# Performance work log

Hardware: AMD Instinct MI355X
Metric: run time of the kernel (lower is better)

## Reference

```python
import jax, jax.numpy as jnp
import numpy as np

NUM_HEADS = 16
D_MODEL = 1024
NUM_LAYERS = 4
VOCAB = 32000
SEQ_LEN = 1024
BATCH = 4
EPS = 1e-6


def position_embedding(seq_len, d_model):
    pos = jnp.arange(seq_len, dtype=jnp.float32)[:, None]
    i = jnp.arange(d_model, dtype=jnp.float32)[None, :]
    # faithful to source: angle_rates = 1 / (1/10000)^(2*(i//2)/d) = 10000^(2*(i//2)/d)
    angle_rates = jnp.power(10000.0, 2.0 * jnp.floor(i / 2.0) / float(d_model))
    ang = pos * angle_rates  # [S, D]
    return jnp.concatenate([jnp.sin(ang[:, 0::2]), jnp.cos(ang[:, 1::2])], axis=-1)[None]  # [1,S,D]


def layer_norm(x, g, b):
    m = jnp.mean(x, axis=-1, keepdims=True)
    v = jnp.mean(jnp.square(x - m), axis=-1, keepdims=True)
    return (x - m) * jax.lax.rsqrt(v + EPS) * g + b


def setup_inputs() -> dict:
    key = jax.random.key(0)
    ks = jax.random.split(key, 20)
    L, D = NUM_LAYERS, D_MODEL
    s = 0.02
    inp = {
        "x": jax.random.randint(ks[0], (BATCH, SEQ_LEN), 0, VOCAB, dtype=jnp.int32),
        "mask": jnp.zeros((BATCH, 1, 1, SEQ_LEN), dtype=jnp.float32),
        "emb": jax.random.normal(ks[1], (VOCAB, D), dtype=jnp.float32) * s,
        "wq": jax.random.normal(ks[2], (L, D, D), dtype=jnp.float32) * s,
        "bq": jnp.zeros((L, D), dtype=jnp.float32),
        "wk": jax.random.normal(ks[3], (L, D, D), dtype=jnp.float32) * s,
        "bk": jnp.zeros((L, D), dtype=jnp.float32),
        "wv": jax.random.normal(ks[4], (L, D, D), dtype=jnp.float32) * s,
        "bv": jnp.zeros((L, D), dtype=jnp.float32),
        "wo": jax.random.normal(ks[5], (L, D, D), dtype=jnp.float32) * s,
        "bo": jnp.zeros((L, D), dtype=jnp.float32),
        "wf": jax.random.normal(ks[6], (L, D, D), dtype=jnp.float32) * s,
        "bf": jnp.zeros((L, D), dtype=jnp.float32),
        "g1": jnp.ones((L, D), dtype=jnp.float32),
        "b1": jnp.zeros((L, D), dtype=jnp.float32),
        "g2": jnp.ones((L, D), dtype=jnp.float32),
        "b2": jnp.zeros((L, D), dtype=jnp.float32),
    }
    return inp


def encoder_forward(x, mask, emb, wq, bq, wk, bk, wv, bv, wo, bo, wf, bf, g1, b1, g2, b2):
    B, S = x.shape
    D = emb.shape[1]
    H = NUM_HEADS
    dh = D // H
    h = emb[x] * jnp.sqrt(jnp.float32(D))  # [B,S,D]
    h = h + position_embedding(S, D)[:, :S, :]

    def split_heads(t):  # [B,S,D] -> [B,H,S,dh]
        return t.reshape(B, S, H, dh).transpose(0, 2, 1, 3)

    for l in range(wq.shape[0]):
        q = split_heads(h @ wq[l] + bq[l])
        k = split_heads(h @ wk[l] + bk[l])
        v = split_heads(h @ wv[l] + bv[l])
        scores = jnp.einsum("bhqd,bhkd->bhqk", q, k) / jnp.sqrt(jnp.float32(dh))
        scores = scores + mask * -1e9
        w = jax.nn.softmax(scores, axis=-1)
        ctx = jnp.einsum("bhqk,bhkd->bhqd", w, v)  # [B,H,S,dh]
        ctx = ctx.transpose(0, 2, 1, 3).reshape(B, S, D)
        attn_out = ctx @ wo[l] + bo[l]
        h = layer_norm(h + attn_out, g1[l], b1[l])
        ff = h @ wf[l] + bf[l]
        h = layer_norm(h + ff, g2[l], b2[l])
    return h


def reference(x, mask, emb, wq, bq, wk, bk, wv, bv, wo, bo, wf, bf, g1, b1, g2, b2):
    return encoder_forward(x, mask, emb, wq, bq, wk, bk, wv, bv, wo, bo, wf, bf, g1, b1, g2, b2)
```

## Files before the change

kernel.cpp:

```cpp
#include <hip/hip_runtime.h>
#include <hip/hip_bf16.h>
#include <math.h>

typedef __hip_bfloat16 bf16;
typedef unsigned int u32;
typedef __attribute__((ext_vector_type(8))) short short8;
typedef __attribute__((ext_vector_type(4))) float f32x4;


#define ATT_LDK 72
#define PS_LD  72

typedef __attribute__((address_space(3))) u32 lds_u32;
typedef const __attribute__((address_space(1))) u32 glb_u32;
static __device__ __forceinline__ void g2l16(const void* g, void* l) {
    __builtin_amdgcn_global_load_lds((glb_u32*)g, (lds_u32*)l, 16, 0, 0);
}

static __device__ __forceinline__ unsigned short bf16bits(float f) {
    bf16 h = __float2bfloat16(f);
    return *(unsigned short*)&h;
}

__global__ __launch_bounds__(256) void wprep_kernel(
    const float* __restrict__ wq, const float* __restrict__ wk,
    const float* __restrict__ wv, const float* __restrict__ wo,
    const float* __restrict__ wf, bf16* __restrict__ wt_all)
{
    __shared__ bf16 tile[64][ATT_LDK];
    const int z = blockIdx.z;
    const int l = z / 5, f = z % 5;
    const float* src = (f == 0) ? wq : (f == 1) ? wk : (f == 2) ? wv : (f == 3) ? wo : wf;
    src += (size_t)l * 1024 * 1024;
    bf16* dst = wt_all + ((size_t)l * 5 + f) * 1024 * 1024;

    const int k0 = blockIdx.x * 64, n0 = blockIdx.y * 64;
    const int t = threadIdx.x;
#pragma unroll
    for (int rr = 0; rr < 4; ++rr) {
        int slot = t + rr * 256;
        int r = slot >> 4, c = slot & 15;
        float4 v = *(const float4*)(src + (size_t)(k0 + r) * 1024 + n0 + c * 4);
        tile[c * 4 + 0][r] = __float2bfloat16(v.x);
        tile[c * 4 + 1][r] = __float2bfloat16(v.y);
        tile[c * 4 + 2][r] = __float2bfloat16(v.z);
        tile[c * 4 + 3][r] = __float2bfloat16(v.w);
    }
    __syncthreads();
#pragma unroll
    for (int rr = 0; rr < 2; ++rr) {
        int slot = t + rr * 256;
        int n = slot >> 3, c = slot & 7;
        *(uint4*)(dst + (size_t)(n0 + n) * 1024 + k0 + c * 8) = *(const uint4*)&tile[n][c * 8];
    }
}

__global__ void bias_stack_kernel(const float* __restrict__ bq, const float* __restrict__ bk,
                                  const float* __restrict__ bv, float* __restrict__ bqkv)
{
    int i = blockIdx.x * 256 + threadIdx.x;
    if (i < 4 * 3072) {
        int l = i / 3072, c = i % 3072;
        int fam = c >> 10, cc = c & 1023;
        const float* s = (fam == 0) ? bq : (fam == 1) ? bk : bv;
        bqkv[i] = s[l * 1024 + cc];
    }
}

__global__ __launch_bounds__(256) void pe_kernel(float* __restrict__ pe)
{
    int idx = blockIdx.x * 256 + threadIdx.x;
    int d0 = (idx & 255) * 4;
    int s = idx >> 8;
    float out[4];
#pragma unroll
    for (int j = 0; j < 4; ++j) {
        int d = d0 + j;
        int m = (d < 512) ? d : (d - 512);
        float ex = (float)(2 * m) * (1.0f / 1024.0f);
        float rate = (float)pow(10000.0, (double)ex);
        float ang = (float)s * rate;
        double a = (double)ang;
        out[j] = (d < 512) ? (float)sin(a) : (float)cos(a);
    }
    *(float4*)(pe + (size_t)s * 1024 + d0) = *(float4*)out;
}

__global__ __launch_bounds__(256) void embed_kernel(
    const int* __restrict__ x, const float* __restrict__ emb,
    const float* __restrict__ pe,
    float* __restrict__ hf, bf16* __restrict__ hb)
{
    int idx = blockIdx.x * 256 + threadIdx.x;
    int d0 = (idx & 255) * 4;
    int row = idx >> 8;
    int s = row & 1023;
    int tok = x[row];
    float4 e = *(const float4*)(emb + (size_t)tok * 1024 + d0);
    float4 p = *(const float4*)(pe + (size_t)s * 1024 + d0);
    float out[4] = {e.x * 32.0f + p.x, e.y * 32.0f + p.y,
                    e.z * 32.0f + p.z, e.w * 32.0f + p.w};
    *(float4*)(hf + (size_t)row * 1024 + d0) = *(float4*)out;
    unsigned short pk[4];
#pragma unroll
    for (int j = 0; j < 4; ++j) pk[j] = bf16bits(out[j]);
    *(uint2*)(hb + (size_t)row * 1024 + d0) = *(uint2*)pk;
}

__global__ __launch_bounds__(256, 3) void gemm_bt_kernel(
    const bf16* __restrict__ A, const bf16* __restrict__ Bt,
    const float* __restrict__ bias,
    bf16* __restrict__ Cb, bf16* __restrict__ VtOut,
    int M, int N, int K)
{
    __shared__ bf16 As[2][128 * 32];
    __shared__ bf16 Bs[2][128 * 32];
    __shared__ bf16 Cst[4][16 * PS_LD];
    const int t = threadIdx.x;
    const int lane = t & 63, wave = t >> 6;
    const int wr = wave >> 1, wc = wave & 1;
    const int lidx = lane & 15, quad = lane >> 4;
    const int m0 = blockIdx.x * 128, n0 = blockIdx.y * 128;

    f32x4 acc[4][4];
#pragma unroll
    for (int i = 0; i < 4; ++i)
#pragma unroll
        for (int j = 0; j < 4; ++j) acc[i][j] = (f32x4){0.f, 0.f, 0.f, 0.f};

    const int r0 = wave * 32;
    const int rloc = lane >> 2;
    const int csw = ((lane & 3) ^ ((lane >> 3) & 3)) * 8;
    const bf16* Abase = A  + (size_t)(m0 + r0 + rloc) * K + csw;
    const bf16* Bbase = Bt + (size_t)(n0 + r0 + rloc) * K + csw;
    const int lofs = r0 * 32;
    const int aslot = (quad ^ ((lidx >> 1) & 3)) * 8;

    g2l16(Abase,                  &As[0][lofs]);
    g2l16(Abase + 16 * (size_t)K, &As[0][lofs + 16 * 32]);
    g2l16(Bbase,                  &Bs[0][lofs]);
    g2l16(Bbase + 16 * (size_t)K, &Bs[0][lofs + 16 * 32]);

    for (int k0 = 0; k0 < K; k0 += 32) {
        __syncthreads();
        const int cur = (k0 >> 5) & 1;
        if (k0 + 32 < K) {
            const int kn = k0 + 32;
            g2l16(Abase + kn,                  &As[cur ^ 1][lofs]);
            g2l16(Abase + kn + 16 * (size_t)K, &As[cur ^ 1][lofs + 16 * 32]);
            g2l16(Bbase + kn,                  &Bs[cur ^ 1][lofs]);
            g2l16(Bbase + kn + 16 * (size_t)K, &Bs[cur ^ 1][lofs + 16 * 32]);
        }

        short8 af[4], bfr[4];
#pragma unroll
        for (int i = 0; i < 4; ++i)
            af[i] = *(const short8*)(&As[cur][(wr * 64 + i * 16 + lidx) * 32 + aslot]);
#pragma unroll
        for (int j = 0; j < 4; ++j)
            bfr[j] = *(const short8*)(&Bs[cur][(wc * 64 + j * 16 + lidx) * 32 + aslot]);
#pragma unroll
        for (int i = 0; i < 4; ++i)
#pragma unroll
            for (int j = 0; j < 4; ++j)
                acc[i][j] = __builtin_amdgcn_mfma_f32_16x16x32_bf16(af[i], bfr[j], acc[i][j], 0, 0, 0);
    }

    float bvj[4];
#pragma unroll
    for (int j = 0; j < 4; ++j)
        bvj[j] = bias ? bias[n0 + wc * 64 + j * 16 + lidx] : 0.0f;

    if (VtOut && n0 >= 2048) {
        const int bidx = m0 >> 10;
        const int s_base = (m0 & 1023) + wr * 64 + quad * 4;
        const int d_base = (n0 - 2048) + wc * 64;
#pragma unroll
        for (int i = 0; i < 4; ++i)
#pragma unroll
            for (int j = 0; j < 4; ++j) {
                unsigned short pk[4];
#pragma unroll
                for (int r = 0; r < 4; ++r)
                    pk[r] = bf16bits(acc[i][j][r] + bvj[j]);
                bf16* dst = VtOut + ((size_t)bidx * 1024 + d_base + j * 16 + lidx) * 1024
                            + s_base + i * 16;
                *(uint2*)dst = *(const uint2*)pk;
            }
    } else {
        const int row16 = lane >> 2, c4 = lane & 3;
#pragma unroll
        for (int i = 0; i < 4; ++i) {
#pragma unroll
            for (int j = 0; j < 4; ++j)
#pragma unroll
                for (int r = 0; r < 4; ++r)
                    Cst[wave][(quad * 4 + r) * PS_LD + j * 16 + lidx] =
                        __float2bfloat16(acc[i][j][r] + bvj[j]);
            bf16* dst = Cb + (size_t)(m0 + wr * 64 + i * 16 + row16) * N + n0 + wc * 64;
            const bf16* srcr = &Cst[wave][row16 * PS_LD];
#pragma unroll
            for (int h = 0; h < 2; ++h)
                *(uint4*)(dst + (c4 + 4 * h) * 8) = *(const uint4*)(srcr + (c4 + 4 * h) * 8);
        }
    }
}

__global__ __launch_bounds__(256, 4) void gemm64_kernel(
    const bf16* __restrict__ A, const bf16* __restrict__ Bt,
    const float* __restrict__ bias, const float* __restrict__ resid,
    float* __restrict__ Cf,
    int M, int N, int K)
{
    __shared__ bf16 As[2][64 * 32];
    __shared__ bf16 Bs[2][128 * 32];
    const int t = threadIdx.x;
    const int lane = t & 63, wave = t >> 6;
    const int wr = wave >> 1, wc = wave & 1;
    const int lidx = lane & 15, quad = lane >> 4;
    const int m0 = blockIdx.x * 64, n0 = blockIdx.y * 128;

    f32x4 acc[2][4];
#pragma unroll
    for (int i = 0; i < 2; ++i)
#pragma unroll
        for (int j = 0; j < 4; ++j) acc[i][j] = (f32x4){0.f, 0.f, 0.f, 0.f};

    const int rloc = lane >> 2;
    const int csw = ((lane & 3) ^ ((lane >> 3) & 3)) * 8;
    const bf16* Abase = A  + (size_t)(m0 + wave * 16 + rloc) * K + csw;
    const bf16* Bbase = Bt + (size_t)(n0 + wave * 32 + rloc) * K + csw;
    const int alofs = wave * 16 * 32;
    const int blofs = wave * 32 * 32;
    const int aslot = (quad ^ ((lidx >> 1) & 3)) * 8;

    g2l16(Abase,                  &As[0][alofs]);
    g2l16(Bbase,                  &Bs[0][blofs]);
    g2l16(Bbase + 16 * (size_t)K, &Bs[0][blofs + 16 * 32]);

    for (int k0 = 0; k0 < K; k0 += 32) {
        __syncthreads();
        const int cur = (k0 >> 5) & 1;
        if (k0 + 32 < K) {
            const int kn = k0 + 32;
            g2l16(Abase + kn,                  &As[cur ^ 1][alofs]);
            g2l16(Bbase + kn,                  &Bs[cur ^ 1][blofs]);
            g2l16(Bbase + kn + 16 * (size_t)K, &Bs[cur ^ 1][blofs + 16 * 32]);
        }

        short8 af[2], bfr[4];
#pragma unroll
        for (int i = 0; i < 2; ++i)
            af[i] = *(const short8*)(&As[cur][(wr * 32 + i * 16 + lidx) * 32 + aslot]);
#pragma unroll
        for (int j = 0; j < 4; ++j)
            bfr[j] = *(const short8*)(&Bs[cur][(wc * 64 + j * 16 + lidx) * 32 + aslot]);
#pragma unroll
        for (int i = 0; i < 2; ++i)
#pragma unroll
            for (int j = 0; j < 4; ++j)
                acc[i][j] = __builtin_amdgcn_mfma_f32_16x16x32_bf16(af[i], bfr[j], acc[i][j], 0, 0, 0);
    }

#pragma unroll
    for (int i = 0; i < 2; ++i)
#pragma unroll
        for (int j = 0; j < 4; ++j) {
            int col = n0 + wc * 64 + j * 16 + lidx;
            float bv = bias[col];
#pragma unroll
            for (int r = 0; r < 4; ++r) {
                int rowg = m0 + wr * 32 + i * 16 + quad * 4 + r;
                Cf[(size_t)rowg * N + col] =
                    acc[i][j][r] + bv + resid[(size_t)rowg * N + col];
            }
        }
}

__global__ __launch_bounds__(512, 4) void attention_kernel(
    const bf16* __restrict__ QKV,
    const bf16* __restrict__ Vt,
    const float* __restrict__ mask,
    bf16* __restrict__ ctx)
{
    __shared__ bf16 Ks[2][64 * 64];
    __shared__ bf16 Vs[2][64 * 64];
    __shared__ bf16 Ps[8][16 * PS_LD];

    const int t = threadIdx.x, lane = t & 63, wave = t >> 6;
    const int quad = lane >> 4, lidx = lane & 15;
    const int b = blockIdx.x >> 4, hh = blockIdx.x & 15;
    const int q0 = blockIdx.y * 128 + wave * 16;

    const int r8 = lane >> 3;
    const int gc = ((lane & 7) ^ r8) * 8;
    const bf16* kg0 = QKV + (size_t)(b * 1024 + wave * 8 + r8) * 3072 + 1024 + hh * 64 + gc;
    const bf16* vg0 = Vt  + (size_t)(b * 1024 + hh * 64 + wave * 8 + r8) * 1024 + gc;
    const int lofs = wave * 8 * 64;

    short8 qf[2];
    {
        const bf16* qp = QKV + (size_t)(b * 1024 + q0 + lidx) * 3072 + hh * 64;
        qf[0] = *(const short8*)(qp + quad * 8);
        qf[1] = *(const short8*)(qp + 32 + quad * 8);
    }

    f32x4 Oacc[4];
#pragma unroll
    for (int nt = 0; nt < 4; ++nt) Oacc[nt] = (f32x4){0.f, 0.f, 0.f, 0.f};
    float psum[4] = {0.f, 0.f, 0.f, 0.f};

    const int fslot = lidx & 7;

    g2l16(kg0, &Ks[0][lofs]);
    g2l16(vg0, &Vs[0][lofs]);

    for (int kt = 0; kt < 16; ++kt) {
        __syncthreads();
        const int cur = kt & 1;
        if (kt < 15) {
            g2l16(kg0 + (size_t)(kt + 1) * 64 * 3072, &Ks[cur ^ 1][lofs]);
            g2l16(vg0 + (kt + 1) * 64,                &Vs[cur ^ 1][lofs]);
        }

        f32x4 sacc[4];
#pragma unroll
        for (int nt = 0; nt < 4; ++nt) sacc[nt] = (f32x4){0.f, 0.f, 0.f, 0.f};
#pragma unroll
        for (int kk = 0; kk < 2; ++kk)
#pragma unroll
            for (int nt = 0; nt < 4; ++nt) {
                short8 kf = *(const short8*)(&Ks[cur][(nt * 16 + lidx) * 64 + (((kk * 4 + quad) ^ fslot) * 8)]);
                sacc[nt] = __builtin_amdgcn_mfma_f32_16x16x32_bf16(qf[kk], kf, sacc[nt], 0, 0, 0);
            }

#pragma unroll
        for (int nt = 0; nt < 4; ++nt) {
            float mv = mask[b * 1024 + kt * 64 + nt * 16 + lidx] * -1e9f;
#pragma unroll
            for (int r = 0; r < 4; ++r) {
                float p = __expf(sacc[nt][r] * 0.125f + mv);
                sacc[nt][r] = p;
                psum[r] += p;
            }
        }

#pragma unroll
        for (int nt = 0; nt < 4; ++nt)
#pragma unroll
            for (int r = 0; r < 4; ++r)
                Ps[wave][(quad * 4 + r) * PS_LD + nt * 16 + lidx] = __float2bfloat16(sacc[nt][r]);

#pragma unroll
        for (int kk = 0; kk < 2; ++kk) {
            short8 pf = *(const short8*)(&Ps[wave][lidx * PS_LD + kk * 32 + quad * 8]);
#pragma unroll
            for (int nt = 0; nt < 4; ++nt) {
                short8 vf = *(const short8*)(&Vs[cur][(nt * 16 + lidx) * 64 + (((kk * 4 + quad) ^ fslot) * 8)]);
                Oacc[nt] = __builtin_amdgcn_mfma_f32_16x16x32_bf16(pf, vf, Oacc[nt], 0, 0, 0);
            }
        }
    }

#pragma unroll
    for (int off = 1; off < 16; off <<= 1)
#pragma unroll
        for (int r = 0; r < 4; ++r)
            psum[r] += __shfl_xor(psum[r], off, 64);
    float linv[4];
#pragma unroll
    for (int r = 0; r < 4; ++r) linv[r] = 1.0f / psum[r];

#pragma unroll
    for (int nt = 0; nt < 4; ++nt)
#pragma unroll
        for (int r = 0; r < 4; ++r)
            Ps[wave][(quad * 4 + r) * PS_LD + nt * 16 + lidx] = __float2bfloat16(Oacc[nt][r] * linv[r]);

    const int row16 = lane >> 2, c4 = lane & 3;
    bf16* dst = ctx + (size_t)(b * 1024 + q0 + row16) * 1024 + hh * 64;
    const bf16* srcr = &Ps[wave][row16 * PS_LD];
#pragma unroll
    for (int h = 0; h < 2; ++h)
        *(uint4*)(dst + (c4 + 4 * h) * 8) = *(const uint4*)(srcr + (c4 + 4 * h) * 8);
}

__global__ __launch_bounds__(256) void add_ln_kernel(
    const float* __restrict__ x,
    const float* __restrict__ g, const float* __restrict__ b,
    float* __restrict__ outf, bf16* __restrict__ outb)
{
    __shared__ float red[4];
    const int row = blockIdx.x;
    const int t = threadIdx.x;
    const int c0 = t * 4;
    float4 xv = *(const float4*)(x + (size_t)row * 1024 + c0);
    float v[4] = {xv.x, xv.y, xv.z, xv.w};
    float s = v[0] + v[1] + v[2] + v[3];
#pragma unroll
    for (int off = 1; off < 64; off <<= 1) s += __shfl_xor(s, off, 64);
    if ((t & 63) == 0) red[t >> 6] = s;
    __syncthreads();
    float mean = (red[0] + red[1] + red[2] + red[3]) * (1.0f / 1024.0f);
    float sq = 0.f;
#pragma unroll
    for (int i = 0; i < 4; ++i) { float d = v[i] - mean; sq += d * d; }
#pragma unroll
    for (int off = 1; off < 64; off <<= 1) sq += __shfl_xor(sq, off, 64);
    __syncthreads();
    if ((t & 63) == 0) red[t >> 6] = sq;
    __syncthreads();
    float var = (red[0] + red[1] + red[2] + red[3]) * (1.0f / 1024.0f);
    float rs = rsqrtf(var + 1e-6f);
    float4 gv = *(const float4*)(g + c0);
    float4 bv = *(const float4*)(b + c0);
    float gg[4] = {gv.x, gv.y, gv.z, gv.w}, bb[4] = {bv.x, bv.y, bv.z, bv.w};
    float o[4];
    unsigned short pk[4];
#pragma unroll
    for (int i = 0; i < 4; ++i) {
        o[i] = (v[i] - mean) * rs * gg[i] + bb[i];
        pk[i] = bf16bits(o[i]);
    }
    *(float4*)(outf + (size_t)row * 1024 + c0) = *(float4*)o;
    *(uint2*)(outb + (size_t)row * 1024 + c0) = *(uint2*)pk;
}

extern "C" void kernel_launch(void* const* d_in, const int* in_sizes, int n_in,
                              void* d_out, int out_size, void* d_ws, size_t ws_size,
                              hipStream_t stream)
{
    const int*   x    = (const int*)d_in[0];
    const float* mask = (const float*)d_in[1];
    const float* emb  = (const float*)d_in[2];
    const float* wq   = (const float*)d_in[3];
    const float* bq   = (const float*)d_in[4];
    const float* wk   = (const float*)d_in[5];
    const float* bk   = (const float*)d_in[6];
    const float* wv   = (const float*)d_in[7];
    const float* bv   = (const float*)d_in[8];
    const float* wo   = (const float*)d_in[9];
    const float* bo   = (const float*)d_in[10];
    const float* wf   = (const float*)d_in[11];
    const float* bfp  = (const float*)d_in[12];
    const float* g1   = (const float*)d_in[13];
    const float* b1   = (const float*)d_in[14];
    const float* g2   = (const float*)d_in[15];
    const float* b2   = (const float*)d_in[16];

    char* ws = (char*)d_ws;
    float* h_f  = (float*)ws;                 ws += 4096ull * 1024 * 4;
    bf16*  h_b  = (bf16*)ws;                  ws += 4096ull * 1024 * 2;
    bf16*  qkv  = (bf16*)ws;                  ws += 4096ull * 3072 * 2;
    bf16*  vt   = (bf16*)ws;                  ws += 4096ull * 1024 * 2;
    bf16*  ctx  = (bf16*)ws;                  ws += 4096ull * 1024 * 2;
    bf16*  wt   = (bf16*)ws;                  ws += 20ull * 1024 * 1024 * 2;
    float* pe   = (float*)ws;                 ws += 1024ull * 1024 * 4;
    float* bqkv = (float*)ws;                 ws += 4ull * 3072 * 4;
    float* delta = (float*)qkv;

    wprep_kernel<<<dim3(16, 16, 20), 256, 0, stream>>>(wq, wk, wv, wo, wf, wt);
    bias_stack_kernel<<<dim3(48), 256, 0, stream>>>(bq, bk, bv, bqkv);
    pe_kernel<<<dim3(1024), 256, 0, stream>>>(pe);
    embed_kernel<<<dim3(4096), 256, 0, stream>>>(x, emb, pe, h_f, h_b);

    for (int l = 0; l < 4; ++l) {
        bf16* wt_l = wt + (size_t)l * 5 * 1024 * 1024;
        gemm_bt_kernel<<<dim3(32, 24), 256, 0, stream>>>(
            h_b, wt_l, bqkv + l * 3072, qkv, vt, 4096, 3072, 1024);
        attention_kernel<<<dim3(64, 8), 512, 0, stream>>>(qkv, vt, mask, ctx);
        gemm64_kernel<<<dim3(64, 8), 256, 0, stream>>>(
            ctx, wt_l + 3ull * 1024 * 1024, bo + l * 1024, h_f, delta, 4096, 1024, 1024);
        add_ln_kernel<<<dim3(4096), 256, 0, stream>>>(
            delta, g1 + l * 1024, b1 + l * 1024, h_f, h_b);
        gemm64_kernel<<<dim3(64, 8), 256, 0, stream>>>(
            h_b, wt_l + 4ull * 1024 * 1024, bfp + l * 1024, h_f, delta, 4096, 1024, 1024);
        float* outf = (l == 3) ? (float*)d_out : h_f;
        add_ln_kernel<<<dim3(4096), 256, 0, stream>>>(
            delta, g2 + l * 1024, b2 + l * 1024, outf, h_b);
    }
    (void)in_sizes; (void)n_in; (void)out_size; (void)ws_size;
}
```

Baseline: 774.9 us.

## Replace QKV GEMM with 256x256-tile, 4-stage pipelined kernel and grid swizzle

```diff
diff --git a/kernel.cpp b/kernel.cpp
--- a/kernel.cpp
+++ b/kernel.cpp
@@ -107,76 +107,105 @@
     *(uint2*)(hb + (size_t)row * 1024 + d0) = *(uint2*)pk;
 }
 
-__global__ __launch_bounds__(256, 3) void gemm_bt_kernel(
+#define BAR() asm volatile("s_barrier" ::: "memory")
+#define VM6() asm volatile("s_waitcnt vmcnt(6)" ::: "memory")
+
+__global__ __launch_bounds__(512, 2) void gemm256_kernel(
     const bf16* __restrict__ A, const bf16* __restrict__ Bt,
     const float* __restrict__ bias,
-    bf16* __restrict__ Cb, bf16* __restrict__ VtOut,
-    int M, int N, int K)
-{
-    __shared__ bf16 As[2][128 * 32];
-    __shared__ bf16 Bs[2][128 * 32];
-    __shared__ bf16 Cst[4][16 * PS_LD];
+    bf16* __restrict__ Cb, bf16* __restrict__ VtOut)
+{
+    constexpr int K = 1024;
+    constexpr int N = 3072;
+    __shared__ bf16 Asl[4][256 * 32];
+    __shared__ bf16 Bsl[4][256 * 32];
+    __shared__ bf16 Cst[8][16 * PS_LD];
+
     const int t = threadIdx.x;
     const int lane = t & 63, wave = t >> 6;
-    const int wr = wave >> 1, wc = wave & 1;
+    const int wr = wave >> 2, wc = wave & 3;
     const int lidx = lane & 15, quad = lane >> 4;
-    const int m0 = blockIdx.x * 128, n0 = blockIdx.y * 128;
-
-    f32x4 acc[4][4];
-#pragma unroll
-    for (int i = 0; i < 4; ++i)
+
+    const int wg = blockIdx.x;
+    const int swz = (wg & 7) * 24 + (wg >> 3);
+    const int m0 = (swz / 12) * 256;
+    const int n0 = (swz % 12) * 256;
+
+    f32x4 acc[8][4];
+#pragma unroll
+    for (int i = 0; i < 8; ++i)
 #pragma unroll
         for (int j = 0; j < 4; ++j) acc[i][j] = (f32x4){0.f, 0.f, 0.f, 0.f};
 
-    const int r0 = wave * 32;
-    const int rloc = lane >> 2;
+    const int rls = lane >> 2;
     const int csw = ((lane & 3) ^ ((lane >> 3) & 3)) * 8;
-    const bf16* Abase = A  + (size_t)(m0 + r0 + rloc) * K + csw;
-    const bf16* Bbase = Bt + (size_t)(n0 + r0 + rloc) * K + csw;
-    const int lofs = r0 * 32;
+    const bf16* Ag = A  + (size_t)(m0 + wave * 16 + rls) * K + csw;
+    const bf16* Bg = Bt + (size_t)(n0 + wave * 16 + rls) * K + csw;
+    const int lds_lo = (wave * 16) * 32;
+    const int lds_hi = (128 + wave * 16) * 32;
+
+#define STAGE_A(koff, s) do { \
+        g2l16(Ag + (koff), &Asl[s][lds_lo]); \
+        g2l16(Ag + (koff) + 128 * K, &Asl[s][lds_hi]); } while (0)
+#define STAGE_B(koff, s) do { \
+        g2l16(Bg + (koff), &Bsl[s][lds_lo]); \
+        g2l16(Bg + (koff) + 128 * K, &Bsl[s][lds_hi]); } while (0)
+
     const int aslot = (quad ^ ((lidx >> 1) & 3)) * 8;
-
-    g2l16(Abase,                  &As[0][lofs]);
-    g2l16(Abase + 16 * (size_t)K, &As[0][lofs + 16 * 32]);
-    g2l16(Bbase,                  &Bs[0][lofs]);
-    g2l16(Bbase + 16 * (size_t)K, &Bs[0][lofs + 16 * 32]);
-
-    for (int k0 = 0; k0 < K; k0 += 32) {
-        __syncthreads();
-        const int cur = (k0 >> 5) & 1;
-        if (k0 + 32 < K) {
-            const int kn = k0 + 32;
-            g2l16(Abase + kn,                  &As[cur ^ 1][lofs]);
-            g2l16(Abase + kn + 16 * (size_t)K, &As[cur ^ 1][lofs + 16 * 32]);
-            g2l16(Bbase + kn,                  &Bs[cur ^ 1][lofs]);
-            g2l16(Bbase + kn + 16 * (size_t)K, &Bs[cur ^ 1][lofs + 16 * 32]);
-        }
-
-        short8 af[4], bfr[4];
-#pragma unroll
-        for (int i = 0; i < 4; ++i)
-            af[i] = *(const short8*)(&As[cur][(wr * 64 + i * 16 + lidx) * 32 + aslot]);
-#pragma unroll
-        for (int j = 0; j < 4; ++j)
-            bfr[j] = *(const short8*)(&Bs[cur][(wc * 64 + j * 16 + lidx) * 32 + aslot]);
-#pragma unroll
-        for (int i = 0; i < 4; ++i)
-#pragma unroll
-            for (int j = 0; j < 4; ++j)
-                acc[i][j] = __builtin_amdgcn_mfma_f32_16x16x32_bf16(af[i], bfr[j], acc[i][j], 0, 0, 0);
+    const int arow = wr * 128 + lidx;
+    const int brow = wc * 64 + lidx;
+    short8 af[4], bfr[4];
+
+#define READ_A4(s, ib) do { _Pragma("unroll") \
+        for (int ii = 0; ii < 4; ++ii) \
+            af[ii] = *(const short8*)(&Asl[s][(arow + ((ib) + ii) * 16) * 32 + aslot]); } while (0)
+#define READ_B4(s) do { _Pragma("unroll") \
+        for (int jj = 0; jj < 4; ++jj) \
+            bfr[jj] = *(const short8*)(&Bsl[s][(brow + jj * 16) * 32 + aslot]); } while (0)
+
+#define MFMA16(ib) do { \
+        __builtin_amdgcn_s_setprio(1); \
+        _Pragma("unroll") for (int ii = 0; ii < 4; ++ii) \
+        _Pragma("unroll") for (int jj = 0; jj < 4; ++jj) \
+            acc[(ib) + ii][jj] = __builtin_amdgcn_mfma_f32_16x16x32_bf16(af[ii], bfr[jj], acc[(ib) + ii][jj], 0, 0, 0); \
+        __builtin_amdgcn_s_setprio(0); \
+        __builtin_amdgcn_sched_barrier(0); } while (0)
+
+    STAGE_A(0, 0);   STAGE_B(0, 0);
+    STAGE_A(32, 1);  STAGE_B(32, 1);
+    STAGE_A(64, 2);  STAGE_B(64, 2);
+    STAGE_B(96, 3);
+    VM6(); BAR();
+
+    for (int u = 0; u < 8; ++u) {
+        const int kt0 = u * 128;
+        const int kP0 = (kt0 + 96) & 1023;
+        const int kN0 = (kt0 + 128) & 1023;
+        const int kN1 = (kt0 + 160) & 1023;
+        const int kN2 = (kt0 + 192) & 1023;
+        const int kN3 = (kt0 + 224) & 1023;
+
+        READ_A4(0, 0); READ_B4(0); STAGE_A(kP0, 3);          BAR(); MFMA16(0); BAR();
+        READ_A4(0, 4);             STAGE_B(kN0, 0);          BAR(); MFMA16(4); BAR();
+        READ_A4(1, 0); READ_B4(1); STAGE_A(kN0, 0);          BAR(); MFMA16(0); BAR();
+        READ_A4(1, 4);             STAGE_B(kN1, 1);  VM6();  BAR(); MFMA16(4); BAR();
+        READ_A4(2, 0); READ_B4(2); STAGE_A(kN1, 1);          BAR(); MFMA16(0); BAR();
+        READ_A4(2, 4);             STAGE_B(kN2, 2);          BAR(); MFMA16(4); BAR();
+        READ_A4(3, 0); READ_B4(3); STAGE_A(kN2, 2);          BAR(); MFMA16(0); BAR();
+        READ_A4(3, 4);             STAGE_B(kN3, 3);  VM6();  BAR(); MFMA16(4); BAR();
     }
 
     float bvj[4];
 #pragma unroll
     for (int j = 0; j < 4; ++j)
-        bvj[j] = bias ? bias[n0 + wc * 64 + j * 16 + lidx] : 0.0f;
-
-    if (VtOut && n0 >= 2048) {
+        bvj[j] = bias[n0 + wc * 64 + j * 16 + lidx];
+
+    if (n0 >= 2048) {
         const int bidx = m0 >> 10;
-        const int s_base = (m0 & 1023) + wr * 64 + quad * 4;
         const int d_base = (n0 - 2048) + wc * 64;
-#pragma unroll
-        for (int i = 0; i < 4; ++i)
+        const int s_base = (m0 & 1023) + wr * 128 + quad * 4;
+#pragma unroll
+        for (int i = 0; i < 8; ++i)
 #pragma unroll
             for (int j = 0; j < 4; ++j) {
                 unsigned short pk[4];
@@ -190,20 +219,25 @@
     } else {
         const int row16 = lane >> 2, c4 = lane & 3;
 #pragma unroll
-        for (int i = 0; i < 4; ++i) {
+        for (int i = 0; i < 8; ++i) {
 #pragma unroll
             for (int j = 0; j < 4; ++j)
 #pragma unroll
                 for (int r = 0; r < 4; ++r)
                     Cst[wave][(quad * 4 + r) * PS_LD + j * 16 + lidx] =
                         __float2bfloat16(acc[i][j][r] + bvj[j]);
-            bf16* dst = Cb + (size_t)(m0 + wr * 64 + i * 16 + row16) * N + n0 + wc * 64;
+            bf16* dst = Cb + (size_t)(m0 + wr * 128 + i * 16 + row16) * N + n0 + wc * 64;
             const bf16* srcr = &Cst[wave][row16 * PS_LD];
 #pragma unroll
             for (int h = 0; h < 2; ++h)
                 *(uint4*)(dst + (c4 + 4 * h) * 8) = *(const uint4*)(srcr + (c4 + 4 * h) * 8);
         }
     }
+#undef STAGE_A
+#undef STAGE_B
+#undef READ_A4
+#undef READ_B4
+#undef MFMA16
 }
 
 __global__ __launch_bounds__(256, 4) void gemm64_kernel(
@@ -466,8 +500,8 @@
 
     for (int l = 0; l < 4; ++l) {
         bf16* wt_l = wt + (size_t)l * 5 * 1024 * 1024;
-        gemm_bt_kernel<<<dim3(32, 24), 256, 0, stream>>>(
-            h_b, wt_l, bqkv + l * 3072, qkv, vt, 4096, 3072, 1024);
+        gemm256_kernel<<<dim3(192), 512, 0, stream>>>(
+            h_b, wt_l, bqkv + l * 3072, qkv, vt);
         attention_kernel<<<dim3(64, 8), 512, 0, stream>>>(qkv, vt, mask, ctx);
         gemm64_kernel<<<dim3(64, 8), 256, 0, stream>>>(
             ctx, wt_l + 3ull * 1024 * 1024, bo + l * 1024, h_f, delta, 4096, 1024, 1024);
```

Result: slower. 791.2 us (+2.1%).

## Load V fragments directly from global, stage mask in LDS, precompute PE rates

Applied to the files above, without the earlier changes.

```diff
diff --git a/kernel.cpp b/kernel.cpp
--- a/kernel.cpp
+++ b/kernel.cpp
@@ -56,9 +56,15 @@
 }
 
 __global__ void bias_stack_kernel(const float* __restrict__ bq, const float* __restrict__ bk,
-                                  const float* __restrict__ bv, float* __restrict__ bqkv)
+                                  const float* __restrict__ bv, float* __restrict__ bqkv,
+                                  float* __restrict__ rate)
 {
     int i = blockIdx.x * 256 + threadIdx.x;
+    if (i < 1024) {
+        int m = (i < 512) ? i : (i - 512);
+        float ex = (float)(2 * m) * (1.0f / 1024.0f);
+        rate[i] = (float)pow(10000.0, (double)ex);
+    }
     if (i < 4 * 3072) {
         int l = i / 3072, c = i % 3072;
         int fam = c >> 10, cc = c & 1023;
@@ -67,7 +73,8 @@
     }
 }
 
-__global__ __launch_bounds__(256) void pe_kernel(float* __restrict__ pe)
+__global__ __launch_bounds__(256) void pe_kernel(const float* __restrict__ rate,
+                                                 float* __restrict__ pe)
 {
     int idx = blockIdx.x * 256 + threadIdx.x;
     int d0 = (idx & 255) * 4;
@@ -76,10 +83,7 @@
 #pragma unroll
     for (int j = 0; j < 4; ++j) {
         int d = d0 + j;
-        int m = (d < 512) ? d : (d - 512);
-        float ex = (float)(2 * m) * (1.0f / 1024.0f);
-        float rate = (float)pow(10000.0, (double)ex);
-        float ang = (float)s * rate;
+        float ang = (float)s * rate[d];
         double a = (double)ang;
         out[j] = (d < 512) ? (float)sin(a) : (float)cos(a);
     }
@@ -284,8 +288,8 @@
     bf16* __restrict__ ctx)
 {
     __shared__ bf16 Ks[2][64 * 64];
-    __shared__ bf16 Vs[2][64 * 64];
     __shared__ bf16 Ps[8][16 * PS_LD];
+    __shared__ float Ms[1024];
 
     const int t = threadIdx.x, lane = t & 63, wave = t >> 6;
     const int quad = lane >> 4, lidx = lane & 15;
@@ -295,8 +299,10 @@
     const int r8 = lane >> 3;
     const int gc = ((lane & 7) ^ r8) * 8;
     const bf16* kg0 = QKV + (size_t)(b * 1024 + wave * 8 + r8) * 3072 + 1024 + hh * 64 + gc;
-    const bf16* vg0 = Vt  + (size_t)(b * 1024 + hh * 64 + wave * 8 + r8) * 1024 + gc;
     const int lofs = wave * 8 * 64;
+
+    Ms[t]       = mask[b * 1024 + t] * -1e9f;
+    Ms[t + 512] = mask[b * 1024 + t + 512] * -1e9f;
 
     short8 qf[2];
     {
@@ -305,6 +311,8 @@
         qf[1] = *(const short8*)(qp + 32 + quad * 8);
     }
 
+    const bf16* vbase = Vt + (size_t)(b * 1024 + hh * 64) * 1024;
+
     f32x4 Oacc[4];
 #pragma unroll
     for (int nt = 0; nt < 4; ++nt) Oacc[nt] = (f32x4){0.f, 0.f, 0.f, 0.f};
@@ -313,15 +321,12 @@
     const int fslot = lidx & 7;
 
     g2l16(kg0, &Ks[0][lofs]);
-    g2l16(vg0, &Vs[0][lofs]);
 
     for (int kt = 0; kt < 16; ++kt) {
         __syncthreads();
         const int cur = kt & 1;
-        if (kt < 15) {
+        if (kt < 15)
             g2l16(kg0 + (size_t)(kt + 1) * 64 * 3072, &Ks[cur ^ 1][lofs]);
-            g2l16(vg0 + (kt + 1) * 64,                &Vs[cur ^ 1][lofs]);
-        }
 
         f32x4 sacc[4];
 #pragma unroll
@@ -336,7 +341,7 @@
 
 #pragma unroll
         for (int nt = 0; nt < 4; ++nt) {
-            float mv = mask[b * 1024 + kt * 64 + nt * 16 + lidx] * -1e9f;
+            float mv = Ms[kt * 64 + nt * 16 + lidx];
 #pragma unroll
             for (int r = 0; r < 4; ++r) {
                 float p = __expf(sacc[nt][r] * 0.125f + mv);
@@ -356,7 +361,8 @@
             short8 pf = *(const short8*)(&Ps[wave][lidx * PS_LD + kk * 32 + quad * 8]);
 #pragma unroll
             for (int nt = 0; nt < 4; ++nt) {
-                short8 vf = *(const short8*)(&Vs[cur][(nt * 16 + lidx) * 64 + (((kk * 4 + quad) ^ fslot) * 8)]);
+                short8 vf = *(const short8*)(vbase + (size_t)(nt * 16 + lidx) * 1024
+                                             + kt * 64 + kk * 32 + quad * 8);
                 Oacc[nt] = __builtin_amdgcn_mfma_f32_16x16x32_bf16(pf, vf, Oacc[nt], 0, 0, 0);
             }
         }
@@ -457,11 +463,12 @@
     bf16*  wt   = (bf16*)ws;                  ws += 20ull * 1024 * 1024 * 2;
     float* pe   = (float*)ws;                 ws += 1024ull * 1024 * 4;
     float* bqkv = (float*)ws;                 ws += 4ull * 3072 * 4;
+    float* rate = (float*)ws;                 ws += 1024ull * 4;
     float* delta = (float*)qkv;
 
     wprep_kernel<<<dim3(16, 16, 20), 256, 0, stream>>>(wq, wk, wv, wo, wf, wt);
-    bias_stack_kernel<<<dim3(48), 256, 0, stream>>>(bq, bk, bv, bqkv);
-    pe_kernel<<<dim3(1024), 256, 0, stream>>>(pe);
+    bias_stack_kernel<<<dim3(48), 256, 0, stream>>>(bq, bk, bv, bqkv, rate);
+    pe_kernel<<<dim3(1024), 256, 0, stream>>>(rate, pe);
     embed_kernel<<<dim3(4096), 256, 0, stream>>>(x, emb, pe, h_f, h_b);
 
     for (int l = 0; l < 4; ++l) {
```

Result: slower. 877.7 us (+13.3%).
